# Kernel tuning notes

Hardware: AMD Instinct MI355X
Metric: run time of the kernel (lower is better)

## Reference

```python
import jax, jax.numpy as jnp
import numpy as np

HIDDEN = 256
EDGE_DIM = 16
HEADS = 8
HEAD_DIM = HIDDEN // HEADS
B, N = 4, 512


def setup_inputs() -> dict:
    key = jax.random.key(0)
    ks = jax.random.split(key, 16)
    s = 1.0 / np.sqrt(HIDDEN)
    se = 1.0 / np.sqrt(EDGE_DIM)
    return {
        "node_h": jax.random.normal(ks[0], (B, N, HIDDEN), jnp.float32),
        "edge_x": jax.random.normal(ks[1], (B, N, N, EDGE_DIM), jnp.float32),
        "edge_mask": jax.random.randint(ks[2], (B, N, N), 0, 2, jnp.int32),
        "Wq": jax.random.normal(ks[3], (HIDDEN, HIDDEN), jnp.float32) * s,
        "bq": jnp.zeros((HIDDEN,), jnp.float32),
        "Wk": jax.random.normal(ks[4], (HIDDEN, HIDDEN), jnp.float32) * s,
        "bk": jnp.zeros((HIDDEN,), jnp.float32),
        "Wv": jax.random.normal(ks[5], (HIDDEN, HIDDEN), jnp.float32) * s,
        "bv": jnp.zeros((HIDDEN,), jnp.float32),
        "We1": jax.random.normal(ks[6], (EDGE_DIM, HIDDEN), jnp.float32) * se,
        "be1": jnp.zeros((HIDDEN,), jnp.float32),
        "We2": jax.random.normal(ks[7], (HIDDEN, HEADS), jnp.float32) * s,
        "be2": jnp.zeros((HEADS,), jnp.float32),
        "Wo": jax.random.normal(ks[8], (HIDDEN, HIDDEN), jnp.float32) * s,
        "bo": jnp.zeros((HIDDEN,), jnp.float32),
        "ln_g": jnp.ones((HIDDEN,), jnp.float32),
        "ln_b": jnp.zeros((HIDDEN,), jnp.float32),
    }


def reference(node_h, edge_x, edge_mask, Wq, bq, Wk, bk, Wv, bv,
              We1, be1, We2, be2, Wo, bo, ln_g, ln_b):
    Bsz, Nn, _ = node_h.shape
    # projections -> [B, H, N, D]
    def heads(x):
        return x.reshape(Bsz, Nn, HEADS, HEAD_DIM).transpose(0, 2, 1, 3)
    q = heads(node_h @ Wq + bq)
    k = heads(node_h @ Wk + bk)
    v = heads(node_h @ Wv + bv)

    scores = jnp.einsum('bhid,bhjd->bhij', q, k) / np.sqrt(HEAD_DIM)
    scores = jax.nn.leaky_relu(scores, negative_slope=0.2)

    # edge bias MLP: [B,N,N,E] -> [B,N,N,H] -> [B,H,N,N]
    eb = jax.nn.relu(edge_x @ We1 + be1) @ We2 + be2
    scores = scores + eb.transpose(0, 3, 1, 2)

    valid = (edge_mask != 0) | jnp.eye(Nn, dtype=bool)[None]  # [B,N,N]
    scores = jnp.where(valid[:, None], scores, -1e9)

    attn = jax.nn.softmax(scores, axis=-1)
    out = jnp.einsum('bhij,bhjd->bhid', attn, v)
    out = out.transpose(0, 2, 1, 3).reshape(Bsz, Nn, HIDDEN)
    out = out @ Wo + bo

    x = node_h + out
    mu = jnp.mean(x, axis=-1, keepdims=True)
    var = jnp.var(x, axis=-1, keepdims=True)
    x = (x - mu) / jnp.sqrt(var + 1e-5) * ln_g + ln_b
    return jax.nn.relu(x), attn
```

## Files before the change

kernel.cpp:

```cpp
#include <hip/hip_runtime.h>

#define BATCH 4
#define NN 512
#define HID 256
#define EDIM 16
#define HEADS 8
#define HDIM 32

typedef __attribute__((ext_vector_type(8))) short bf16x8;
typedef __attribute__((ext_vector_type(4))) float f32x4;

__device__ inline unsigned short bf16_hi(float x){ return (unsigned short)(__float_as_uint(x)>>16); }
__device__ inline float bf16_f(unsigned short s){ return __uint_as_float(((unsigned)s)<<16); }
__device__ inline unsigned short bf16_rn(float x){
    unsigned u = __float_as_uint(x);
    unsigned r = u + 0x7FFFu + ((u>>16)&1u);
    return (unsigned short)(r>>16);
}
__device__ inline unsigned cvt_pk_bf16(float a, float b){
    unsigned d;
    asm("v_cvt_pk_bf16_f32 %0, %1, %2" : "=v"(d) : "v"(a), "v"(b));
    return d;
}
__device__ inline void hilo8(float4 A, float4 B, bf16x8& hi, bf16x8& lo){
    float xs[8] = {A.x,A.y,A.z,A.w,B.x,B.y,B.z,B.w};
    unsigned hu[4], lu[4];
#pragma unroll
    for (int p = 0; p < 4; ++p){
        unsigned u0 = __float_as_uint(xs[2*p]), u1 = __float_as_uint(xs[2*p+1]);
        float h0 = __uint_as_float(u0 & 0xFFFF0000u);
        float h1 = __uint_as_float(u1 & 0xFFFF0000u);
        hu[p] = (u0 >> 16) | (u1 & 0xFFFF0000u);
        lu[p] = cvt_pk_bf16(xs[2*p] - h0, xs[2*p+1] - h1);
    }
    int4 hv; hv.x = hu[0]; hv.y = hu[1]; hv.z = hu[2]; hv.w = hu[3];
    int4 lv; lv.x = lu[0]; lv.y = lu[1]; lv.z = lu[2]; lv.w = lu[3];
    hi = *(bf16x8*)&hv; lo = *(bf16x8*)&lv;
}

__global__ void k_pack(const float* __restrict__ We1, const float* __restrict__ be1,
                       const float* __restrict__ We2,
                       unsigned short* __restrict__ W1P, unsigned short* __restrict__ W2P) {
    int t = threadIdx.x;
#pragma unroll
    for (int rep = 0; rep < 4; ++rep) {
        int p = rep * 256 + t;
        int ut = p >> 6, lane = p & 63;
        int q = lane >> 4, r = lane & 15;
        int unit = ut * 16 + r;
#pragma unroll
        for (int j = 0; j < 8; ++j) {
            int k = q * 8 + j;
            unsigned short ov;
            if (k < 16) ov = bf16_hi(We1[k * HID + unit]);
            else if (k < 31) {
                float v = We1[(k - 16) * HID + unit];
                ov = bf16_rn(v - bf16_f(bf16_hi(v)));
            } else ov = bf16_rn(be1[unit]);
            W1P[p * 8 + j] = ov;
        }
    }
#pragma unroll
    for (int rep = 0; rep < 2; ++rep) {
        int p = rep * 256 + t;
        int kt = p >> 6, lane = p & 63;
        int q = lane >> 4, r = lane & 15;
#pragma unroll
        for (int jj = 0; jj < 8; ++jj) {
            int unit = kt * 32 + q * 8 + jj;
            W2P[p * 8 + jj] = (r < 8) ? bf16_rn(We2[unit * HEADS + r]) : (unsigned short)0;
        }
    }
}

__global__ __launch_bounds__(256) void k_qkv(
    const float* __restrict__ node_h,
    const float* __restrict__ Wq, const float* __restrict__ bq,
    const float* __restrict__ Wk, const float* __restrict__ bk,
    const float* __restrict__ Wv, const float* __restrict__ bv,
    float* __restrict__ q, float* __restrict__ k, float* __restrict__ vT) {
    int blk = blockIdx.x;
    int b = blk >> 7, i0 = (blk & 127) << 2;
    int t = threadIdx.x;
    __shared__ __align__(16) float s_h[4][HID];
#pragma unroll
    for (int u = 0; u < 4; ++u)
        s_h[u][t] = node_h[((size_t)b * NN + i0 + u) * HID + t];
    __syncthreads();
    float aq[4], ak[4], av[4];
    float bqv = bq[t], bkv = bk[t], bvv = bv[t];
#pragma unroll
    for (int u = 0; u < 4; ++u) { aq[u] = bqv; ak[u] = bkv; av[u] = bvv; }
#pragma unroll 4
    for (int rr = 0; rr < HID; ++rr) {
        float wq = Wq[rr * HID + t], wk = Wk[rr * HID + t], wv = Wv[rr * HID + t];
#pragma unroll
        for (int u = 0; u < 4; ++u) {
            float x = s_h[u][rr];
            aq[u] = fmaf(x, wq, aq[u]);
            ak[u] = fmaf(x, wk, ak[u]);
            av[u] = fmaf(x, wv, av[u]);
        }
    }
    int h = t >> 5, d = t & 31;
#pragma unroll
    for (int u = 0; u < 4; ++u) {
        size_t idx = ((size_t)(b * HEADS + h) * NN + i0 + u) * HDIM + d;
        q[idx] = aq[u]; k[idx] = ak[u];
        vT[((size_t)(b * HEADS + h) * HDIM + d) * NN + i0 + u] = av[u];
    }
}

__global__ __launch_bounds__(256, 4) void k_eb(
    const float* __restrict__ edge_x,
    const unsigned short* __restrict__ W1P, const unsigned short* __restrict__ W2P,
    const float* __restrict__ be2, float* __restrict__ eb) {
    int bid = blockIdx.x;
    int b = bid >> 8, i0 = ((bid >> 1) & 127) << 2, jh = bid & 1;
    int t = threadIdx.x;
    int w = t >> 6, lane = t & 63;
    int q2 = lane >> 4, r = lane & 15;

    __shared__ __align__(16) char s_hb[4][2048];

    bf16x8 W1Pr[16];
#pragma unroll
    for (int ut = 0; ut < 16; ++ut)
        W1Pr[ut] = *(const bf16x8*)(W1P + ((size_t)ut * 64 + lane) * 8);
    bf16x8 w2f[8];
#pragma unroll
    for (int kt = 0; kt < 8; ++kt)
        w2f[kt] = *(const bf16x8*)(W2P + ((size_t)kt * 64 + lane) * 8);
    float be2r = (r < 8) ? be2[r] : 0.f;

    size_t xbase = (((size_t)b * NN + i0 + w) * NN) * EDIM + (size_t)((q2 & 1) * 8);
    char* hb = &s_hb[w][0];
    const f32x4 zero4 = {0.f, 0.f, 0.f, 0.f};
    for (int c = 0; c < 16; ++c) {
        int cc = jh * 16 + c;
        const float4* px = (const float4*)(edge_x + xbase + (size_t)(cc * 16 + r) * EDIM);
        float4 x0 = px[0], x1 = px[1];
        unsigned u0 = cvt_pk_bf16(x0.x, x0.y);
        unsigned u1 = cvt_pk_bf16(x0.z, x0.w);
        unsigned u2 = cvt_pk_bf16(x1.x, x1.y);
        unsigned u3 = cvt_pk_bf16(x1.z, x1.w);
        if (q2 == 3) u3 = (u3 & 0xFFFFu) | 0x3F800000u;
        int4 bxi; bxi.x = u0; bxi.y = u1; bxi.z = u2; bxi.w = u3;
        bf16x8 bx = *(bf16x8*)&bxi;

        f32x4 acc = {be2r, be2r, be2r, be2r};
#pragma unroll
        for (int qt = 0; qt < 4; ++qt) {
#pragma unroll
            for (int u2i = 0; u2i < 4; ++u2i) {
                int ut = qt * 4 + u2i;
                f32x4 ch = __builtin_amdgcn_mfma_f32_16x16x32_bf16(W1Pr[ut], bx, zero4, 0, 0, 0);
                unsigned p01 = cvt_pk_bf16(fmaxf(ch[0], 0.f), fmaxf(ch[1], 0.f));
                unsigned p23 = cvt_pk_bf16(fmaxf(ch[2], 0.f), fmaxf(ch[3], 0.f));
                int ktl = (ut >> 1) & 1;
                unsigned off = (unsigned)(ktl * 1024 + (16 * ((ut & 1) * 2 + (q2 >> 1)) + r) * 16 + (q2 & 1) * 8);
                uint2 wv; wv.x = p01; wv.y = p23;
                *(uint2*)(hb + off) = wv;
            }
#pragma unroll
            for (int k2 = 0; k2 < 2; ++k2) {
                bf16x8 af = *(const bf16x8*)(hb + k2 * 1024 + lane * 16);
                acc = __builtin_amdgcn_mfma_f32_16x16x32_bf16(af, w2f[qt * 2 + k2], acc, 0, 0, 0);
            }
        }
        if (r < 8)
            *(f32x4*)(eb + (((size_t)(b * HEADS + r) * NN) + (i0 + w)) * NN + cc * 16 + q2 * 4) = acc;
    }
}

__global__ __launch_bounds__(256, 3) void k_attn2(
    const int* __restrict__ emask,
    const float* __restrict__ q, const float* __restrict__ k, const float* __restrict__ vT,
    float* attn, float* __restrict__ ao) {
    int bid = blockIdx.x;
    int b = bid >> 8, h = (bid >> 5) & 7, ic = bid & 31;
    int i0 = ic << 4;
    int t = threadIdx.x, w = t >> 6, lane = t & 63;
    int q2 = lane >> 4, r = lane & 15;
    size_t bh = (size_t)b * HEADS + h;

    __shared__ __align__(16) float s_sc[16][516];
    __shared__ __align__(16) unsigned short s_ab[16][520];
    __shared__ float s_out[2][16][33];

    bf16x8 qhi, qlo;
    {
        const float4* qp = (const float4*)(q + ((bh * NN) + i0 + r) * HDIM + q2 * 8);
        hilo8(qp[0], qp[1], qhi, qlo);
    }

    const float scale = 0.17677669529663687f;
    for (int c = 0; c < 8; ++c) {
        int jt = w * 8 + c;
        bf16x8 khi, klo;
        {
            const float4* kp = (const float4*)(k + (bh * NN + jt * 16 + r) * HDIM + q2 * 8);
            hilo8(kp[0], kp[1], khi, klo);
        }
        f32x4 cc = {0.f, 0.f, 0.f, 0.f};
        cc = __builtin_amdgcn_mfma_f32_16x16x32_bf16(qhi, khi, cc, 0, 0, 0);
        cc = __builtin_amdgcn_mfma_f32_16x16x32_bf16(qhi, klo, cc, 0, 0, 0);
        cc = __builtin_amdgcn_mfma_f32_16x16x32_bf16(qlo, khi, cc, 0, 0, 0);
        int j = jt * 16 + r;
#pragma unroll
        for (int reg = 0; reg < 4; ++reg) {
            int row = q2 * 4 + reg;
            int i = i0 + row;
            float s = cc[reg] * scale;
            s = s > 0.f ? s : 0.2f * s;
            s += attn[(bh * NN + i) * NN + j];
            bool valid = (emask[((size_t)b * NN + i) * NN + j] != 0) || (j == i);
            s_sc[row][j] = valid ? s : -1e9f;
        }
    }
    __syncthreads();

#pragma unroll
    for (int rr = 0; rr < 4; ++rr) {
        int row = w * 4 + rr;
        f32x4 v0 = *(f32x4*)&s_sc[row][lane * 8];
        f32x4 v1 = *(f32x4*)&s_sc[row][lane * 8 + 4];
        float mx = fmaxf(fmaxf(fmaxf(v0[0], v0[1]), fmaxf(v0[2], v0[3])),
                         fmaxf(fmaxf(v1[0], v1[1]), fmaxf(v1[2], v1[3])));
#pragma unroll
        for (int off = 32; off > 0; off >>= 1) mx = fmaxf(mx, __shfl_xor(mx, off));
        float e[8];
        e[0] = __expf(v0[0] - mx); e[1] = __expf(v0[1] - mx);
        e[2] = __expf(v0[2] - mx); e[3] = __expf(v0[3] - mx);
        e[4] = __expf(v1[0] - mx); e[5] = __expf(v1[1] - mx);
        e[6] = __expf(v1[2] - mx); e[7] = __expf(v1[3] - mx);
        float sum = ((e[0] + e[1]) + (e[2] + e[3])) + ((e[4] + e[5]) + (e[6] + e[7]));
#pragma unroll
        for (int off = 32; off > 0; off >>= 1) sum += __shfl_xor(sum, off);
        float inv = 1.f / sum;
#pragma unroll
        for (int l = 0; l < 8; ++l) e[l] *= inv;
        float* arow = attn + (bh * NN + i0 + row) * NN + lane * 8;
        float4 o0; o0.x = e[0]; o0.y = e[1]; o0.z = e[2]; o0.w = e[3];
        float4 o1; o1.x = e[4]; o1.y = e[5]; o1.z = e[6]; o1.w = e[7];
        *(float4*)(arow) = o0;
        *(float4*)(arow + 4) = o1;
        uint4 pk;
        pk.x = cvt_pk_bf16(e[0], e[1]); pk.y = cvt_pk_bf16(e[2], e[3]);
        pk.z = cvt_pk_bf16(e[4], e[5]); pk.w = cvt_pk_bf16(e[6], e[7]);
        *(uint4*)((char*)s_ab + row * 1040 + lane * 16) = pk;
    }
    __syncthreads();

    {
        int part = w >> 1, nh = w & 1;
        const float* vbase = vT + (bh * HDIM + nh * 16 + r) * NN;
        f32x4 acc = {0.f, 0.f, 0.f, 0.f};
        for (int kt = 0; kt < 16; ++kt) {
            bf16x8 af = *(bf16x8*)((char*)s_ab + r * 1040 + kt * 64 + q2 * 16);
            const float4* vp = (const float4*)(vbase + kt * 32 + q2 * 8);
            float4 x0 = vp[0], x1 = vp[1];
            float xs[8] = {x0.x, x0.y, x0.z, x0.w, x1.x, x1.y, x1.z, x1.w};
            bf16x8 bfg;
            if (part == 0) {
                unsigned hu[4];
#pragma unroll
                for (int p = 0; p < 4; ++p) {
                    unsigned a0 = __float_as_uint(xs[2*p]), a1 = __float_as_uint(xs[2*p+1]);
                    hu[p] = (a0 >> 16) | (a1 & 0xFFFF0000u);
                }
                int4 hv; hv.x = hu[0]; hv.y = hu[1]; hv.z = hu[2]; hv.w = hu[3];
                bfg = *(bf16x8*)&hv;
            } else {
                unsigned lu[4];
#pragma unroll
                for (int p = 0; p < 4; ++p) {
                    unsigned a0 = __float_as_uint(xs[2*p]), a1 = __float_as_uint(xs[2*p+1]);
                    float h0 = __uint_as_float(a0 & 0xFFFF0000u);
                    float h1 = __uint_as_float(a1 & 0xFFFF0000u);
                    lu[p] = cvt_pk_bf16(xs[2*p] - h0, xs[2*p+1] - h1);
                }
                int4 lv; lv.x = lu[0]; lv.y = lu[1]; lv.z = lu[2]; lv.w = lu[3];
                bfg = *(bf16x8*)&lv;
            }
            acc = __builtin_amdgcn_mfma_f32_16x16x32_bf16(af, bfg, acc, 0, 0, 0);
        }
#pragma unroll
        for (int reg = 0; reg < 4; ++reg)
            s_out[part][q2 * 4 + reg][nh * 16 + r] = acc[reg];
    }
    __syncthreads();

#pragma unroll
    for (int rep = 0; rep < 2; ++rep) {
        int idx = rep * 256 + t;
        int row = idx >> 5, d = idx & 31;
        ao[((size_t)b * NN + i0 + row) * HID + h * HDIM + d] =
            s_out[0][row][d] + s_out[1][row][d];
    }
}

__global__ __launch_bounds__(256) void k_final(
    const float* __restrict__ ao, const float* __restrict__ node_h,
    const float* __restrict__ Wo, const float* __restrict__ bo,
    const float* __restrict__ ln_g, const float* __restrict__ ln_b,
    float* __restrict__ out) {
    int blk = blockIdx.x;
    size_t bi0 = (size_t)blk * 4;
    int t = threadIdx.x;
    __shared__ __align__(16) float s_a[4][HID];
    __shared__ float s_red[4][4][2];
#pragma unroll
    for (int u = 0; u < 4; ++u)
        s_a[u][t] = ao[(bi0 + u) * HID + t];
    __syncthreads();
    float bov = bo[t];
    float o[4];
#pragma unroll
    for (int u = 0; u < 4; ++u) o[u] = bov;
#pragma unroll 4
    for (int rr = 0; rr < HID; ++rr) {
        float wo = Wo[rr * HID + t];
#pragma unroll
        for (int u = 0; u < 4; ++u) o[u] = fmaf(s_a[u][rr], wo, o[u]);
    }
    float g = ln_g[t], bb = ln_b[t];
    int wave = t >> 6, ln = t & 63;
    float x[4];
#pragma unroll
    for (int u = 0; u < 4; ++u) {
        x[u] = node_h[(bi0 + u) * HID + t] + o[u];
        float s1 = x[u], s2 = x[u] * x[u];
#pragma unroll
        for (int off = 32; off > 0; off >>= 1) { s1 += __shfl_xor(s1, off); s2 += __shfl_xor(s2, off); }
        if (ln == 0) { s_red[u][wave][0] = s1; s_red[u][wave][1] = s2; }
    }
    __syncthreads();
#pragma unroll
    for (int u = 0; u < 4; ++u) {
        float s1 = s_red[u][0][0] + s_red[u][1][0] + s_red[u][2][0] + s_red[u][3][0];
        float s2 = s_red[u][0][1] + s_red[u][1][1] + s_red[u][2][1] + s_red[u][3][1];
        float mean = s1 * (1.f / HID);
        float var = s2 * (1.f / HID) - mean * mean;
        float inv = rsqrtf(var + 1e-5f);
        float y = (x[u] - mean) * inv * g + bb;
        out[(bi0 + u) * HID + t] = fmaxf(y, 0.f);
    }
}

extern "C" void kernel_launch(void* const* d_in, const int* in_sizes, int n_in,
                              void* d_out, int out_size, void* d_ws, size_t ws_size,
                              hipStream_t stream) {
    const float* node_h = (const float*)d_in[0];
    const float* edge_x = (const float*)d_in[1];
    const int*   emask  = (const int*)d_in[2];
    const float* Wq = (const float*)d_in[3];
    const float* bq = (const float*)d_in[4];
    const float* Wk = (const float*)d_in[5];
    const float* bk = (const float*)d_in[6];
    const float* Wv = (const float*)d_in[7];
    const float* bv = (const float*)d_in[8];
    const float* We1 = (const float*)d_in[9];
    const float* be1 = (const float*)d_in[10];
    const float* We2 = (const float*)d_in[11];
    const float* be2 = (const float*)d_in[12];
    const float* Wo = (const float*)d_in[13];
    const float* bo = (const float*)d_in[14];
    const float* ln_g = (const float*)d_in[15];
    const float* ln_b = (const float*)d_in[16];

    float* out_x  = (float*)d_out;
    float* out_at = (float*)d_out + (size_t)BATCH * NN * HID;

    float* ws = (float*)d_ws;
    float* q    = ws;
    float* kbuf = ws + 524288;
    float* vT   = ws + 1048576;
    float* ao   = ws + 1572864;
    unsigned short* W1P = (unsigned short*)(ws + 2097152);
    unsigned short* W2P = W1P + 8192;

    const int NBI = BATCH * NN;

    hipLaunchKernelGGL(k_pack, dim3(1), dim3(256), 0, stream, We1, be1, We2, W1P, W2P);
    hipLaunchKernelGGL(k_qkv, dim3(NBI / 4), dim3(256), 0, stream,
                       node_h, Wq, bq, Wk, bk, Wv, bv, q, kbuf, vT);
    hipLaunchKernelGGL(k_eb, dim3(1024), dim3(256), 0, stream,
                       edge_x, W1P, W2P, be2, out_at);
    hipLaunchKernelGGL(k_attn2, dim3(1024), dim3(256), 0, stream,
                       emask, q, kbuf, vT, out_at, ao);
    hipLaunchKernelGGL(k_final, dim3(NBI / 4), dim3(256), 0, stream,
                       ao, node_h, Wo, bo, ln_g, ln_b, out_x);
}
```

Measured before the change: 147.3 us.

## Replace LDS round-trip in edge-bias MLP with cross-lane permlane swaps

The edge-bias kernel no longer writes the ReLU'd hidden activations to shared memory and reads them back as MFMA A-fragments. It now reshuffles two adjacent MFMA outputs in registers with v_permlane32/16_swap so they form the operand of the second MFMA directly. The grid is also split across four j-quarters instead of two, doubling block count, and launch bounds are lowered to 3 waves per EU. This removes LDS traffic and the write-read dependency, at the risk of a wrong lane mapping if the permlane layout does not match the previous LDS layout, plus more redundant loading of the weight registers per block.

```diff
diff --git a/kernel.cpp b/kernel.cpp
--- a/kernel.cpp
+++ b/kernel.cpp
@@ -111,18 +111,16 @@
     }
 }
 
-__global__ __launch_bounds__(256, 4) void k_eb(
+__global__ __launch_bounds__(256, 3) void k_eb(
     const float* __restrict__ edge_x,
     const unsigned short* __restrict__ W1P, const unsigned short* __restrict__ W2P,
     const float* __restrict__ be2, float* __restrict__ eb) {
     int bid = blockIdx.x;
-    int b = bid >> 8, i0 = ((bid >> 1) & 127) << 2, jh = bid & 1;
+    int b = bid >> 9, i0 = ((bid >> 2) & 127) << 2, jq = bid & 3;
     int t = threadIdx.x;
     int w = t >> 6, lane = t & 63;
     int q2 = lane >> 4, r = lane & 15;
 
-    __shared__ __align__(16) char s_hb[4][2048];
-
     bf16x8 W1Pr[16];
 #pragma unroll
     for (int ut = 0; ut < 16; ++ut)
@@ -134,10 +132,9 @@
     float be2r = (r < 8) ? be2[r] : 0.f;
 
     size_t xbase = (((size_t)b * NN + i0 + w) * NN) * EDIM + (size_t)((q2 & 1) * 8);
-    char* hb = &s_hb[w][0];
     const f32x4 zero4 = {0.f, 0.f, 0.f, 0.f};
-    for (int c = 0; c < 16; ++c) {
-        int cc = jh * 16 + c;
+    for (int c = 0; c < 8; ++c) {
+        int cc = jq * 8 + c;
         const float4* px = (const float4*)(edge_x + xbase + (size_t)(cc * 16 + r) * EDIM);
         float4 x0 = px[0], x1 = px[1];
         unsigned u0 = cvt_pk_bf16(x0.x, x0.y);
@@ -152,20 +149,20 @@
 #pragma unroll
         for (int qt = 0; qt < 4; ++qt) {
 #pragma unroll
-            for (int u2i = 0; u2i < 4; ++u2i) {
-                int ut = qt * 4 + u2i;
-                f32x4 ch = __builtin_amdgcn_mfma_f32_16x16x32_bf16(W1Pr[ut], bx, zero4, 0, 0, 0);
-                unsigned p01 = cvt_pk_bf16(fmaxf(ch[0], 0.f), fmaxf(ch[1], 0.f));
-                unsigned p23 = cvt_pk_bf16(fmaxf(ch[2], 0.f), fmaxf(ch[3], 0.f));
-                int ktl = (ut >> 1) & 1;
-                unsigned off = (unsigned)(ktl * 1024 + (16 * ((ut & 1) * 2 + (q2 >> 1)) + r) * 16 + (q2 & 1) * 8);
-                uint2 wv; wv.x = p01; wv.y = p23;
-                *(uint2*)(hb + off) = wv;
-            }
-#pragma unroll
-            for (int k2 = 0; k2 < 2; ++k2) {
-                bf16x8 af = *(const bf16x8*)(hb + k2 * 1024 + lane * 16);
-                acc = __builtin_amdgcn_mfma_f32_16x16x32_bf16(af, w2f[qt * 2 + k2], acc, 0, 0, 0);
+            for (int pr = 0; pr < 2; ++pr) {
+                int ut0 = qt * 4 + pr * 2;
+                f32x4 c0 = __builtin_amdgcn_mfma_f32_16x16x32_bf16(W1Pr[ut0],     bx, zero4, 0, 0, 0);
+                f32x4 c1 = __builtin_amdgcn_mfma_f32_16x16x32_bf16(W1Pr[ut0 + 1], bx, zero4, 0, 0, 0);
+                unsigned P0 = cvt_pk_bf16(fmaxf(c0[0], 0.f), fmaxf(c0[1], 0.f));
+                unsigned P1 = cvt_pk_bf16(fmaxf(c0[2], 0.f), fmaxf(c0[3], 0.f));
+                unsigned Q0 = cvt_pk_bf16(fmaxf(c1[0], 0.f), fmaxf(c1[1], 0.f));
+                unsigned Q1 = cvt_pk_bf16(fmaxf(c1[2], 0.f), fmaxf(c1[3], 0.f));
+                asm("v_permlane32_swap_b32 %0, %1" : "+v"(P0), "+v"(Q0));
+                asm("v_permlane16_swap_b32 %0, %1" : "+v"(P0), "+v"(Q0));
+                asm("v_permlane32_swap_b32 %0, %1" : "+v"(P1), "+v"(Q1));
+                asm("v_permlane16_swap_b32 %0, %1" : "+v"(P1), "+v"(Q1));
+                int4 ai; ai.x = (int)P0; ai.y = (int)P1; ai.z = (int)Q0; ai.w = (int)Q1;
+                acc = __builtin_amdgcn_mfma_f32_16x16x32_bf16(*(bf16x8*)&ai, w2f[qt * 2 + pr], acc, 0, 0, 0);
             }
         }
         if (r < 8)
@@ -385,7 +382,7 @@
     hipLaunchKernelGGL(k_pack, dim3(1), dim3(256), 0, stream, We1, be1, We2, W1P, W2P);
     hipLaunchKernelGGL(k_qkv, dim3(NBI / 4), dim3(256), 0, stream,
                        node_h, Wq, bq, Wk, bk, Wv, bv, q, kbuf, vT);
-    hipLaunchKernelGGL(k_eb, dim3(1024), dim3(256), 0, stream,
+    hipLaunchKernelGGL(k_eb, dim3(2048), dim3(256), 0, stream,
                        edge_x, W1P, W2P, be2, out_at);
     hipLaunchKernelGGL(k_attn2, dim3(1024), dim3(256), 0, stream,
                        emask, q, kbuf, vT, out_at, ao);
```

Result: no change. 148.5 us (+0.8%).
